# Optimization experiments

Measured on AMD Instinct MI355X. Metric: run time of the kernel, lower is better.

## Reference

```python
import jax, jax.numpy as jnp
import numpy as np

EPS = 1e-8

def _gauss_kernel(ks=7, sigma=7.0/6.0):
    x = np.arange(ks, dtype=np.float32) - ks // 2
    g = np.exp(-0.5 * (x / sigma) ** 2)
    g = g / g.sum()
    k = np.outer(g, g).astype(np.float32)
    return jnp.asarray(k.reshape(1, 1, ks, ks))

GK = _gauss_kernel()
SOBEL_X = jnp.asarray(np.array([[1, 0, -1], [2, 0, -2], [1, 0, -1]], dtype=np.float32).reshape(1, 1, 3, 3))
SOBEL_Y = jnp.transpose(SOBEL_X, (0, 1, 3, 2))


def _conv(x, k, pad):
    return jax.lax.conv_general_dilated(
        x, k, window_strides=(1, 1), padding=[(pad, pad), (pad, pad)],
        dimension_numbers=('NCHW', 'OIHW', 'NCHW'))


def _mscn(g):
    mu = _conv(g, GK, 3)
    sigma = jnp.sqrt(jnp.abs(_conv(g * g, GK, 3) - mu * mu + EPS))
    return (g - mu) / (sigma + EPS)


def _grad_mag(g):
    gx = _conv(g, SOBEL_X, 1)
    gy = _conv(g, SOBEL_Y, 1)
    return jnp.sqrt(gx * gx + gy * gy + EPS)


def _frfsim(D, R):
    w = jnp.array([0.2989, 0.587, 0.114], dtype=D.dtype).reshape(1, 3, 1, 1)
    Dg = jnp.sum(D * w, axis=1, keepdims=True)  # (B,1,H,W)
    Rg = jnp.sum(R * w, axis=1, keepdims=True)

    # per-sample SSIM-like constants from dynamic range of Dg (calculate_C)
    d = (jnp.max(Dg, axis=(2, 3), keepdims=True) -
         jnp.min(Dg, axis=(2, 3), keepdims=True))  # (B,1,1,1)
    CM = (0.01 * d) ** 2
    CD = CM / 2.0
    CG = (0.03 * d) ** 2
    CC = CG / 2.0

    # MSCN structure map
    Dm = _mscn(Dg)
    Rm = _mscn(Rg)
    SM = (2 * Dm * Rm + CM) / (Dm ** 2 + Rm ** 2 + CM)

    # dark-channel map
    Ddc = jnp.min(D, axis=1, keepdims=True) / 255.0
    Rdc = jnp.min(R, axis=1, keepdims=True) / 255.0
    SD = (2 * Ddc * Rdc + CD) / (Ddc ** 2 + Rdc ** 2 + CD + EPS)
    mean_SD = jnp.mean(SD, axis=(1, 2, 3))  # (B,)

    # HSV color map: s = (max-min+eps)/(max+eps), v = max, color = s*v
    def color(x):
        mx = jnp.max(x, axis=1, keepdims=True)
        mn = jnp.min(x, axis=1, keepdims=True)
        return ((mx - mn + EPS) / (mx + EPS)) * mx
    Dc = color(D)
    Rc = color(R)
    SC = (2 * Dc * Rc + CC) / (Dc ** 2 + Rc ** 2 + CC + EPS)

    # Sobel gradient map
    Dgr = _grad_mag(Dg)
    Rgr = _grad_mag(Rg)
    SG = (2 * Dgr * Rgr + CG) / (Dgr ** 2 + Rgr ** 2 + CG + EPS)

    # adaptive exponents from mean dark-channel similarity
    t1 = 0.85
    b1 = jnp.where((mean_SD > t1) & (mean_SD <= 1.0), 0.2,
                   jnp.where((mean_SD >= 0.0) & (mean_SD <= t1), 0.8, 0.5))
    b2 = jnp.where((mean_SD > t1) & (mean_SD <= 1.0), 0.8,
                   jnp.where((mean_SD >= 0.0) & (mean_SD <= t1), 0.2, 0.5))
    b1 = b1.astype(D.dtype).reshape(-1, 1, 1, 1)
    b2 = b2.astype(D.dtype).reshape(-1, 1, 1, 1)

    # safe_pow(base, b) == |base|^b (complex pow of |base|+0j, real part)
    frfsimmap = jnp.power(jnp.abs(SM * SD), b1) * jnp.power(SG * SC, b2)
    frfsimval = jnp.mean(jnp.abs(frfsimmap), axis=(1, 2, 3))  # (B,)
    return jnp.mean(frfsimval)  # == sum_i frfsimval_i / B


def setup_inputs() -> dict:
    key = jax.random.key(0)
    kD, kR = jax.random.split(key)
    B, H, W = 32, 512, 512
    D = jax.random.uniform(kD, (B, 3, H, W), dtype=jnp.float32)
    R = jax.random.uniform(kR, (B, 3, H, W), dtype=jnp.float32)
    return {"D": D, "R": R}


def reference(D, R):
    return _frfsim(D, R)
```

## Files before the change

### kernel.cpp

```cpp
#include <hip/hip_runtime.h>

#define EPSF  1e-8f
#define IMG_W 512
#define IMG_H 512
#define HWPX  (IMG_W*IMG_H)
#define NB    32

#define GW0 0.0125602730f
#define GW1 0.0788280293f
#define GW2 0.2372963577f
#define GW3 0.3426321149f

#define RCPF(x)  __builtin_amdgcn_rcpf(x)
#define SQRTF(x) __builtin_amdgcn_sqrtf(x)
#define LOG2F(x) __builtin_amdgcn_logf(x)
#define EXP2F(x) __builtin_amdgcn_exp2f(x)


__global__ void k_init(unsigned* __restrict__ minb, unsigned* __restrict__ maxb,
                       float* __restrict__ sdsum, float* __restrict__ cand) {
  int t = threadIdx.x;
  if (t < NB) { minb[t] = 0x7F7FFFFFu; maxb[t] = 0u; sdsum[t] = 0.f; }
  if (t < 3*NB) cand[t] = 0.f;
}

__global__ __launch_bounds__(256) void k_minmax(const float* __restrict__ D,
                                                unsigned* __restrict__ minb,
                                                unsigned* __restrict__ maxb) {
  const int b = blockIdx.y, chunk = blockIdx.x, tid = threadIdx.x;
  const float4* P0 = (const float4*)(D + (size_t)b * 3 * HWPX);
  const float4* P1 = P0 + HWPX/4;
  const float4* P2 = P1 + HWPX/4;
  const int i0 = chunk * 512 + tid;
  const int i1 = i0 + 256;
  float4 a0 = P0[i0], c0 = P1[i0], e0 = P2[i0];
  float4 a1 = P0[i1], c1 = P1[i1], e1 = P2[i1];
  float mn = __uint_as_float(0x7F7FFFFFu), mx = 0.f;
  float g;
  g = 0.2989f*a0.x + 0.587f*c0.x + 0.114f*e0.x; mn = fminf(mn,g); mx = fmaxf(mx,g);
  g = 0.2989f*a0.y + 0.587f*c0.y + 0.114f*e0.y; mn = fminf(mn,g); mx = fmaxf(mx,g);
  g = 0.2989f*a0.z + 0.587f*c0.z + 0.114f*e0.z; mn = fminf(mn,g); mx = fmaxf(mx,g);
  g = 0.2989f*a0.w + 0.587f*c0.w + 0.114f*e0.w; mn = fminf(mn,g); mx = fmaxf(mx,g);
  g = 0.2989f*a1.x + 0.587f*c1.x + 0.114f*e1.x; mn = fminf(mn,g); mx = fmaxf(mx,g);
  g = 0.2989f*a1.y + 0.587f*c1.y + 0.114f*e1.y; mn = fminf(mn,g); mx = fmaxf(mx,g);
  g = 0.2989f*a1.z + 0.587f*c1.z + 0.114f*e1.z; mn = fminf(mn,g); mx = fmaxf(mx,g);
  g = 0.2989f*a1.w + 0.587f*c1.w + 0.114f*e1.w; mn = fminf(mn,g); mx = fmaxf(mx,g);
  #pragma unroll
  for (int o = 32; o > 0; o >>= 1) {
    mn = fminf(mn, __shfl_down(mn, o, 64));
    mx = fmaxf(mx, __shfl_down(mx, o, 64));
  }
  __shared__ float smn[4], smx[4];
  if ((tid & 63) == 0) { smn[tid>>6] = mn; smx[tid>>6] = mx; }
  __syncthreads();
  if (tid == 0) {
    mn = fminf(fminf(smn[0],smn[1]), fminf(smn[2],smn[3]));
    mx = fmaxf(fmaxf(smx[0],smx[1]), fmaxf(smx[2],smx[3]));
    atomicMin(minb + b, __float_as_uint(mn));
    atomicMax(maxb + b, __float_as_uint(mx));
  }
}

#define TW 64
#define TH 32
#define HALO 3
#define SWP 72
#define SH  38
#define NCHUNK (SH*18)

__global__ __launch_bounds__(256) void k_main(const float* __restrict__ D, const float* __restrict__ R,
                                              const unsigned* __restrict__ minb,
                                              const unsigned* __restrict__ maxb,
                                              float* __restrict__ sdsum,
                                              float* __restrict__ cand) {
  __shared__ float sDg[SH][SWP];
  __shared__ float sRg[SH][SWP];
  __shared__ float sSD[TH][TW];
  __shared__ float sSC[TH][TW];

  const int tid = threadIdx.x;
  const int b   = blockIdx.z;
  const int tx0 = blockIdx.x * TW;
  const int ty0 = blockIdx.y * TH;

  const float dr = __uint_as_float(maxb[b]) - __uint_as_float(minb[b]);
  const float CM = (0.01f*dr)*(0.01f*dr);
  const float CD = 0.5f*CM;
  const float CG = (0.03f*dr)*(0.03f*dr);
  const float CC = 0.5f*CG;

  const float* D0 = D + (size_t)b*3*HWPX;
  const float* R0 = R + (size_t)b*3*HWPX;
  const float4* fD0 = (const float4*)D0;
  const float4* fD1 = fD0 + HWPX/4;
  const float4* fD2 = fD1 + HWPX/4;
  const float4* fR0 = (const float4*)R0;
  const float4* fR1 = fR0 + HWPX/4;
  const float4* fR2 = fR1 + HWPX/4;

  float sdacc = 0.f;

  const int cx0 = tx0 - 4;
  for (int j = tid; j < NCHUNK; j += 256) {
    const int r  = j / 18;
    const int c  = j - r*18;
    const int gy = ty0 - HALO + r;
    const int gx = cx0 + c*4;
    float4 dg4 = make_float4(0.f,0.f,0.f,0.f);
    float4 rg4 = make_float4(0.f,0.f,0.f,0.f);
    if ((unsigned)gy < IMG_H && gx >= 0 && gx < IMG_W) {
      const int o4 = gy*(IMG_W/4) + (gx >> 2);
      float4 d0 = fD0[o4], d1 = fD1[o4], d2 = fD2[o4];
      float4 r0 = fR0[o4], r1 = fR1[o4], r2 = fR2[o4];
      dg4.x = 0.2989f*d0.x + 0.587f*d1.x + 0.114f*d2.x;
      dg4.y = 0.2989f*d0.y + 0.587f*d1.y + 0.114f*d2.y;
      dg4.z = 0.2989f*d0.z + 0.587f*d1.z + 0.114f*d2.z;
      dg4.w = 0.2989f*d0.w + 0.587f*d1.w + 0.114f*d2.w;
      rg4.x = 0.2989f*r0.x + 0.587f*r1.x + 0.114f*r2.x;
      rg4.y = 0.2989f*r0.y + 0.587f*r1.y + 0.114f*r2.y;
      rg4.z = 0.2989f*r0.z + 0.587f*r1.z + 0.114f*r2.z;
      rg4.w = 0.2989f*r0.w + 0.587f*r1.w + 0.114f*r2.w;
      if (r >= HALO && r < HALO+TH && c >= 1 && c <= 16) {
        float4 sd4, sc4;
        #define MAPS(f) { \
          float dmn = fminf(fminf(d0.f,d1.f),d2.f); \
          float rmn = fminf(fminf(r0.f,r1.f),r2.f); \
          float a_ = dmn*(1.f/255.f), c_ = rmn*(1.f/255.f); \
          float sd = (2.f*a_*c_ + CD) * RCPF(a_*a_ + c_*c_ + CD + EPSF); \
          sd4.f = sd; sdacc += sd; \
          float dmx = fmaxf(fmaxf(d0.f,d1.f),d2.f); \
          float rmx = fmaxf(fmaxf(r0.f,r1.f),r2.f); \
          float dcol = ((dmx-dmn+EPSF) * RCPF(dmx+EPSF)) * dmx; \
          float rcol = ((rmx-rmn+EPSF) * RCPF(rmx+EPSF)) * rmx; \
          sc4.f = (2.f*dcol*rcol + CC) * RCPF(dcol*dcol + rcol*rcol + CC + EPSF); }
        MAPS(x) MAPS(y) MAPS(z) MAPS(w)
        #undef MAPS
        *(float4*)&sSD[r-HALO][(c-1)*4] = sd4;
        *(float4*)&sSC[r-HALO][(c-1)*4] = sc4;
      }
    }
    *(float4*)&sDg[r][c*4] = dg4;
    *(float4*)&sRg[r][c*4] = rg4;
  }
  __syncthreads();

  const int x   = tid & 63;
  const int yo0 = (tid >> 6) * 8;

  float whgD[7]={0}, whqD[7]={0}, whgR[7]={0}, whqR[7]={0};
  float wsxD[5]={0}, wsyD[5]={0}, wsxR[5]={0}, wsyR[5]={0};
  float a0 = 0.f, a1 = 0.f, a2 = 0.f;

  #pragma unroll
  for (int step = 0; step < 14; ++step) {
    const int r = yo0 + step;
    float vD[7], vR[7];
    #pragma unroll
    for (int j = 0; j < 7; ++j) { vD[j] = sDg[r][x+1+j]; vR[j] = sRg[r][x+1+j]; }
    float hgD, hqD, hgR, hqR;
    hgD = GW0*(vD[0]+vD[6]) + GW1*(vD[1]+vD[5]) + GW2*(vD[2]+vD[4]) + GW3*vD[3];
    hgR = GW0*(vR[0]+vR[6]) + GW1*(vR[1]+vR[5]) + GW2*(vR[2]+vR[4]) + GW3*vR[3];
    hqD = GW0*(vD[0]*vD[0]+vD[6]*vD[6]) + GW1*(vD[1]*vD[1]+vD[5]*vD[5])
        + GW2*(vD[2]*vD[2]+vD[4]*vD[4]) + GW3*vD[3]*vD[3];
    hqR = GW0*(vR[0]*vR[0]+vR[6]*vR[6]) + GW1*(vR[1]*vR[1]+vR[5]*vR[5])
        + GW2*(vR[2]*vR[2]+vR[4]*vR[4]) + GW3*vR[3]*vR[3];
    float sxD = vD[2]-vD[4], syD = vD[2]+2.f*vD[3]+vD[4];
    float sxR = vR[2]-vR[4], syR = vR[2]+2.f*vR[3]+vR[4];
    #pragma unroll
    for (int j = 0; j < 6; ++j) {
      whgD[j]=whgD[j+1]; whqD[j]=whqD[j+1]; whgR[j]=whgR[j+1]; whqR[j]=whqR[j+1];
    }
    whgD[6]=hgD; whqD[6]=hqD; whgR[6]=hgR; whqR[6]=hqR;
    #pragma unroll
    for (int j = 0; j < 4; ++j) {
      wsxD[j]=wsxD[j+1]; wsyD[j]=wsyD[j+1]; wsxR[j]=wsxR[j+1]; wsyR[j]=wsyR[j+1];
    }
    wsxD[4]=sxD; wsyD[4]=syD; wsxR[4]=sxR; wsyR[4]=syR;

    if (step >= 6) {
      const int yo = yo0 + step - 6;
      float muD, exD, muR, exR;
      muD = GW0*(whgD[0]+whgD[6]) + GW1*(whgD[1]+whgD[5]) + GW2*(whgD[2]+whgD[4]) + GW3*whgD[3];
      exD = GW0*(whqD[0]+whqD[6]) + GW1*(whqD[1]+whqD[5]) + GW2*(whqD[2]+whqD[4]) + GW3*whqD[3];
      muR = GW0*(whgR[0]+whgR[6]) + GW1*(whgR[1]+whgR[5]) + GW2*(whgR[2]+whgR[4]) + GW3*whgR[3];
      exR = GW0*(whqR[0]+whqR[6]) + GW1*(whqR[1]+whqR[5]) + GW2*(whqR[2]+whqR[4]) + GW3*whqR[3];
      float v0D = sDg[yo+HALO][x+4];
      float v0R = sRg[yo+HALO][x+4];
      float sigD = SQRTF(fabsf(exD - muD*muD + EPSF));
      float sigR = SQRTF(fabsf(exR - muR*muR + EPSF));
      float Dm = (v0D - muD) * RCPF(sigD + EPSF);
      float Rm = (v0R - muR) * RCPF(sigR + EPSF);
      float SM = (2.f*Dm*Rm + CM) * RCPF(Dm*Dm + Rm*Rm + CM);
      float gxD = wsxD[0] + 2.f*wsxD[1] + wsxD[2];
      float gyD = wsyD[0] - wsyD[2];
      float gxR = wsxR[0] + 2.f*wsxR[1] + wsxR[2];
      float gyR = wsyR[0] - wsyR[2];
      float GD = SQRTF(gxD*gxD + gyD*gyD + EPSF);
      float GR = SQRTF(gxR*gxR + gyR*gyR + EPSF);
      float SG = (2.f*GD*GR + CG) * RCPF(GD*GD + GR*GR + CG + EPSF);
      float SDv = sSD[yo][x];
      float SCv = sSC[yo][x];
      float m1 = fabsf(SM * SDv);
      float m2 = SG * SCv;
      float l1 = LOG2F(m1);
      float l2 = LOG2F(m2);
      a0 += EXP2F(0.2f*l1 + 0.8f*l2);
      a1 += EXP2F(0.8f*l1 + 0.2f*l2);
      a2 += EXP2F(0.5f*l1 + 0.5f*l2);
    }
  }

  #pragma unroll
  for (int o = 32; o > 0; o >>= 1) {
    sdacc += __shfl_down(sdacc, o, 64);
    a0    += __shfl_down(a0,    o, 64);
    a1    += __shfl_down(a1,    o, 64);
    a2    += __shfl_down(a2,    o, 64);
  }
  __shared__ float red[4][4];
  const int w = tid >> 6;
  if ((tid & 63) == 0) { red[w][0]=sdacc; red[w][1]=a0; red[w][2]=a1; red[w][3]=a2; }
  __syncthreads();
  if (tid < 4) {
    float t = red[0][tid]+red[1][tid]+red[2][tid]+red[3][tid];
    if (tid == 0) atomicAdd(sdsum + b, t);
    else          atomicAdd(cand + (tid-1)*NB + b, t);
  }
}

__global__ void k_final(const float* __restrict__ sdsum, const float* __restrict__ cand,
                        float* __restrict__ out) {
  const int t = threadIdx.x;
  float v = 0.f;
  if (t < NB) {
    float meanSD = sdsum[t] * (1.f/(float)HWPX);
    float c;
    if      (meanSD > 0.85f && meanSD <= 1.0f)  c = cand[0*NB + t];
    else if (meanSD >= 0.f  && meanSD <= 0.85f) c = cand[1*NB + t];
    else                                        c = cand[2*NB + t];
    v = c;
  }
  #pragma unroll
  for (int o = 32; o > 0; o >>= 1) v += __shfl_down(v, o, 64);
  if (t == 0) out[0] = v * (1.f/8388608.f);
}

extern "C" void kernel_launch(void* const* d_in, const int* in_sizes, int n_in,
                              void* d_out, int out_size, void* d_ws, size_t ws_size,
                              hipStream_t stream) {
  (void)in_sizes; (void)n_in; (void)out_size; (void)ws_size;
  const float* D = (const float*)d_in[0];
  const float* R = (const float*)d_in[1];
  float* out = (float*)d_out;
  unsigned* minb  = (unsigned*)d_ws;
  unsigned* maxb  = minb + NB;
  float*    sdsum = (float*)(maxb + NB);
  float*    cand  = sdsum + NB;

  k_init  <<<1, 128, 0, stream>>>(minb, maxb, sdsum, cand);
  k_minmax<<<dim3(128, NB), 256, 0, stream>>>(D, minb, maxb);
  k_main  <<<dim3(IMG_W/TW, IMG_H/TH, NB), 256, 0, stream>>>(D, R, minb, maxb, sdsum, cand);
  k_final <<<1, 64, 0, stream>>>(sdsum, cand, out);
}
```

Measured before the change: 330.8 us.

## Split D/R stencil passes to cut registers; replace min/max atomics with two-stage reduction

The fused stencil loop that kept D and R sliding windows live together is split into two passes. The first computes the D MSCN values and gradient magnitudes into small per-thread arrays, and the second processes R and combines them. This lowers peak register pressure so more waves can be resident, at the cost of re-reading the D values from shared memory in a separate pass. The per-image min/max atomics are also replaced by per-chunk partial writes plus a small reduction kernel, which adds one extra launch.

```diff
diff --git a/kernel.cpp b/kernel.cpp
--- a/kernel.cpp
+++ b/kernel.cpp
@@ -5,6 +5,7 @@
 #define IMG_H 512
 #define HWPX  (IMG_W*IMG_H)
 #define NB    32
+#define NCHK  128
 
 #define GW0 0.0125602730f
 #define GW1 0.0788280293f
@@ -17,16 +18,15 @@
 #define EXP2F(x) __builtin_amdgcn_exp2f(x)
 
 
-__global__ void k_init(unsigned* __restrict__ minb, unsigned* __restrict__ maxb,
-                       float* __restrict__ sdsum, float* __restrict__ cand) {
+__global__ void k_init(float* __restrict__ sdsum, float* __restrict__ cand) {
   int t = threadIdx.x;
-  if (t < NB) { minb[t] = 0x7F7FFFFFu; maxb[t] = 0u; sdsum[t] = 0.f; }
+  if (t < NB) sdsum[t] = 0.f;
   if (t < 3*NB) cand[t] = 0.f;
 }
 
 __global__ __launch_bounds__(256) void k_minmax(const float* __restrict__ D,
-                                                unsigned* __restrict__ minb,
-                                                unsigned* __restrict__ maxb) {
+                                                float* __restrict__ mnp,
+                                                float* __restrict__ mxp) {
   const int b = blockIdx.y, chunk = blockIdx.x, tid = threadIdx.x;
   const float4* P0 = (const float4*)(D + (size_t)b * 3 * HWPX);
   const float4* P1 = P0 + HWPX/4;
@@ -56,8 +56,27 @@
   if (tid == 0) {
     mn = fminf(fminf(smn[0],smn[1]), fminf(smn[2],smn[3]));
     mx = fmaxf(fmaxf(smx[0],smx[1]), fmaxf(smx[2],smx[3]));
-    atomicMin(minb + b, __float_as_uint(mn));
-    atomicMax(maxb + b, __float_as_uint(mx));
+    mnp[b*NCHK + chunk] = mn;
+    mxp[b*NCHK + chunk] = mx;
+  }
+}
+
+__global__ void k_red(const float* __restrict__ mnp, const float* __restrict__ mxp,
+                      unsigned* __restrict__ minb, unsigned* __restrict__ maxb) {
+  const int b = blockIdx.x, t = threadIdx.x;
+  float mn = mnp[b*NCHK + t];
+  float mx = mxp[b*NCHK + t];
+  #pragma unroll
+  for (int o = 32; o > 0; o >>= 1) {
+    mn = fminf(mn, __shfl_down(mn, o, 64));
+    mx = fmaxf(mx, __shfl_down(mx, o, 64));
+  }
+  __shared__ float smn[2], smx[2];
+  if ((t & 63) == 0) { smn[t>>6] = mn; smx[t>>6] = mx; }
+  __syncthreads();
+  if (t == 0) {
+    minb[b] = __float_as_uint(fminf(smn[0], smn[1]));
+    maxb[b] = __float_as_uint(fmaxf(smx[0], smx[1]));
   }
 }
 
@@ -89,12 +108,10 @@
   const float CG = (0.03f*dr)*(0.03f*dr);
   const float CC = 0.5f*CG;
 
-  const float* D0 = D + (size_t)b*3*HWPX;
-  const float* R0 = R + (size_t)b*3*HWPX;
-  const float4* fD0 = (const float4*)D0;
+  const float4* fD0 = (const float4*)(D + (size_t)b*3*HWPX);
   const float4* fD1 = fD0 + HWPX/4;
   const float4* fD2 = fD1 + HWPX/4;
-  const float4* fR0 = (const float4*)R0;
+  const float4* fR0 = (const float4*)(R + (size_t)b*3*HWPX);
   const float4* fR1 = fR0 + HWPX/4;
   const float4* fR2 = fR1 + HWPX/4;
 
@@ -147,66 +164,91 @@
   const int x   = tid & 63;
   const int yo0 = (tid >> 6) * 8;
 
-  float whgD[7]={0}, whqD[7]={0}, whgR[7]={0}, whqR[7]={0};
-  float wsxD[5]={0}, wsyD[5]={0}, wsxR[5]={0}, wsyR[5]={0};
+  float nD[8], gD[8];
+  {
+    float whg[7]={0,0,0,0,0,0,0}, whq[7]={0,0,0,0,0,0,0};
+    float wsx[3]={0,0,0}, wsy[3]={0,0,0};
+    #pragma unroll
+    for (int st = 0; st < 14; ++st) {
+      const int r = yo0 + st;
+      float v[7];
+      #pragma unroll
+      for (int j = 0; j < 7; ++j) v[j] = sDg[r][x+1+j];
+      float hg = GW0*(v[0]+v[6]) + GW1*(v[1]+v[5]) + GW2*(v[2]+v[4]) + GW3*v[3];
+      float hq = GW0*(v[0]*v[0]+v[6]*v[6]) + GW1*(v[1]*v[1]+v[5]*v[5])
+               + GW2*(v[2]*v[2]+v[4]*v[4]) + GW3*v[3]*v[3];
+      #pragma unroll
+      for (int j = 0; j < 6; ++j) { whg[j]=whg[j+1]; whq[j]=whq[j+1]; }
+      whg[6]=hg; whq[6]=hq;
+      wsx[0]=wsx[1]; wsx[1]=wsx[2]; wsx[2]=v[2]-v[4];
+      wsy[0]=wsy[1]; wsy[1]=wsy[2]; wsy[2]=v[2]+2.f*v[3]+v[4];
+      if (st >= 4 && st < 12) {
+        float gx = wsx[0] + 2.f*wsx[1] + wsx[2];
+        float gy = wsy[0] - wsy[2];
+        gD[st-4] = SQRTF(gx*gx + gy*gy + EPSF);
+      }
+      if (st >= 6) {
+        const int k  = st - 6;
+        const int ya = yo0 + k;
+        float mu = GW0*(whg[0]+whg[6]) + GW1*(whg[1]+whg[5]) + GW2*(whg[2]+whg[4]) + GW3*whg[3];
+        float ex = GW0*(whq[0]+whq[6]) + GW1*(whq[1]+whq[5]) + GW2*(whq[2]+whq[4]) + GW3*whq[3];
+        float v0 = sDg[ya+HALO][x+4];
+        float sig = SQRTF(fabsf(ex - mu*mu + EPSF));
+        nD[k] = (v0 - mu) * RCPF(sig + EPSF);
+      }
+    }
+  }
+
   float a0 = 0.f, a1 = 0.f, a2 = 0.f;
-
-  #pragma unroll
-  for (int step = 0; step < 14; ++step) {
-    const int r = yo0 + step;
-    float vD[7], vR[7];
+  {
+    float whg[7]={0,0,0,0,0,0,0}, whq[7]={0,0,0,0,0,0,0};
+    float wsx[3]={0,0,0}, wsy[3]={0,0,0};
+    float grr[2]={0,0};
     #pragma unroll
-    for (int j = 0; j < 7; ++j) { vD[j] = sDg[r][x+1+j]; vR[j] = sRg[r][x+1+j]; }
-    float hgD, hqD, hgR, hqR;
-    hgD = GW0*(vD[0]+vD[6]) + GW1*(vD[1]+vD[5]) + GW2*(vD[2]+vD[4]) + GW3*vD[3];
-    hgR = GW0*(vR[0]+vR[6]) + GW1*(vR[1]+vR[5]) + GW2*(vR[2]+vR[4]) + GW3*vR[3];
-    hqD = GW0*(vD[0]*vD[0]+vD[6]*vD[6]) + GW1*(vD[1]*vD[1]+vD[5]*vD[5])
-        + GW2*(vD[2]*vD[2]+vD[4]*vD[4]) + GW3*vD[3]*vD[3];
-    hqR = GW0*(vR[0]*vR[0]+vR[6]*vR[6]) + GW1*(vR[1]*vR[1]+vR[5]*vR[5])
-        + GW2*(vR[2]*vR[2]+vR[4]*vR[4]) + GW3*vR[3]*vR[3];
-    float sxD = vD[2]-vD[4], syD = vD[2]+2.f*vD[3]+vD[4];
-    float sxR = vR[2]-vR[4], syR = vR[2]+2.f*vR[3]+vR[4];
-    #pragma unroll
-    for (int j = 0; j < 6; ++j) {
-      whgD[j]=whgD[j+1]; whqD[j]=whqD[j+1]; whgR[j]=whgR[j+1]; whqR[j]=whqR[j+1];
-    }
-    whgD[6]=hgD; whqD[6]=hqD; whgR[6]=hgR; whqR[6]=hqR;
-    #pragma unroll
-    for (int j = 0; j < 4; ++j) {
-      wsxD[j]=wsxD[j+1]; wsyD[j]=wsyD[j+1]; wsxR[j]=wsxR[j+1]; wsyR[j]=wsyR[j+1];
-    }
-    wsxD[4]=sxD; wsyD[4]=syD; wsxR[4]=sxR; wsyR[4]=syR;
-
-    if (step >= 6) {
-      const int yo = yo0 + step - 6;
-      float muD, exD, muR, exR;
-      muD = GW0*(whgD[0]+whgD[6]) + GW1*(whgD[1]+whgD[5]) + GW2*(whgD[2]+whgD[4]) + GW3*whgD[3];
-      exD = GW0*(whqD[0]+whqD[6]) + GW1*(whqD[1]+whqD[5]) + GW2*(whqD[2]+whqD[4]) + GW3*whqD[3];
-      muR = GW0*(whgR[0]+whgR[6]) + GW1*(whgR[1]+whgR[5]) + GW2*(whgR[2]+whgR[4]) + GW3*whgR[3];
-      exR = GW0*(whqR[0]+whqR[6]) + GW1*(whqR[1]+whqR[5]) + GW2*(whqR[2]+whqR[4]) + GW3*whqR[3];
-      float v0D = sDg[yo+HALO][x+4];
-      float v0R = sRg[yo+HALO][x+4];
-      float sigD = SQRTF(fabsf(exD - muD*muD + EPSF));
-      float sigR = SQRTF(fabsf(exR - muR*muR + EPSF));
-      float Dm = (v0D - muD) * RCPF(sigD + EPSF);
-      float Rm = (v0R - muR) * RCPF(sigR + EPSF);
-      float SM = (2.f*Dm*Rm + CM) * RCPF(Dm*Dm + Rm*Rm + CM);
-      float gxD = wsxD[0] + 2.f*wsxD[1] + wsxD[2];
-      float gyD = wsyD[0] - wsyD[2];
-      float gxR = wsxR[0] + 2.f*wsxR[1] + wsxR[2];
-      float gyR = wsyR[0] - wsyR[2];
-      float GD = SQRTF(gxD*gxD + gyD*gyD + EPSF);
-      float GR = SQRTF(gxR*gxR + gyR*gyR + EPSF);
-      float SG = (2.f*GD*GR + CG) * RCPF(GD*GD + GR*GR + CG + EPSF);
-      float SDv = sSD[yo][x];
-      float SCv = sSC[yo][x];
-      float m1 = fabsf(SM * SDv);
-      float m2 = SG * SCv;
-      float l1 = LOG2F(m1);
-      float l2 = LOG2F(m2);
-      a0 += EXP2F(0.2f*l1 + 0.8f*l2);
-      a1 += EXP2F(0.8f*l1 + 0.2f*l2);
-      a2 += EXP2F(0.5f*l1 + 0.5f*l2);
+    for (int st = 0; st < 14; ++st) {
+      const int r = yo0 + st;
+      float v[7];
+      #pragma unroll
+      for (int j = 0; j < 7; ++j) v[j] = sRg[r][x+1+j];
+      float hg = GW0*(v[0]+v[6]) + GW1*(v[1]+v[5]) + GW2*(v[2]+v[4]) + GW3*v[3];
+      float hq = GW0*(v[0]*v[0]+v[6]*v[6]) + GW1*(v[1]*v[1]+v[5]*v[5])
+               + GW2*(v[2]*v[2]+v[4]*v[4]) + GW3*v[3]*v[3];
+      #pragma unroll
+      for (int j = 0; j < 6; ++j) { whg[j]=whg[j+1]; whq[j]=whq[j+1]; }
+      whg[6]=hg; whq[6]=hq;
+      wsx[0]=wsx[1]; wsx[1]=wsx[2]; wsx[2]=v[2]-v[4];
+      wsy[0]=wsy[1]; wsy[1]=wsy[2]; wsy[2]=v[2]+2.f*v[3]+v[4];
+
+      float GRuse = grr[st & 1];
+
+      if (st >= 4 && st < 12) {
+        float gx = wsx[0] + 2.f*wsx[1] + wsx[2];
+        float gy = wsy[0] - wsy[2];
+        grr[st & 1] = SQRTF(gx*gx + gy*gy + EPSF);
+      }
+
+      if (st >= 6) {
+        const int k  = st - 6;
+        const int ya = yo0 + k;
+        float mu = GW0*(whg[0]+whg[6]) + GW1*(whg[1]+whg[5]) + GW2*(whg[2]+whg[4]) + GW3*whg[3];
+        float ex = GW0*(whq[0]+whq[6]) + GW1*(whq[1]+whq[5]) + GW2*(whq[2]+whq[4]) + GW3*whq[3];
+        float v0 = sRg[ya+HALO][x+4];
+        float sig = SQRTF(fabsf(ex - mu*mu + EPSF));
+        float Rm = (v0 - mu) * RCPF(sig + EPSF);
+        float Dm = nD[k];
+        float SM = (2.f*Dm*Rm + CM) * RCPF(Dm*Dm + Rm*Rm + CM);
+        float GDv = gD[k];
+        float SG = (2.f*GDv*GRuse + CG) * RCPF(GDv*GDv + GRuse*GRuse + CG + EPSF);
+        float SDv = sSD[ya][x];
+        float SCv = sSC[ya][x];
+        float m1 = fabsf(SM * SDv);
+        float m2 = SG * SCv;
+        float l1 = LOG2F(m1);
+        float l2 = LOG2F(m2);
+        a0 += EXP2F(0.2f*l1 + 0.8f*l2);
+        a1 += EXP2F(0.8f*l1 + 0.2f*l2);
+        a2 += EXP2F(0.5f*l1 + 0.5f*l2);
+      }
     }
   }
 
@@ -256,9 +298,12 @@
   unsigned* maxb  = minb + NB;
   float*    sdsum = (float*)(maxb + NB);
   float*    cand  = sdsum + NB;
-
-  k_init  <<<1, 128, 0, stream>>>(minb, maxb, sdsum, cand);
-  k_minmax<<<dim3(128, NB), 256, 0, stream>>>(D, minb, maxb);
+  float*    mnp   = cand + 3*NB;
+  float*    mxp   = mnp + NB*NCHK;
+
+  k_init  <<<1, 128, 0, stream>>>(sdsum, cand);
+  k_minmax<<<dim3(NCHK, NB), 256, 0, stream>>>(D, mnp, mxp);
+  k_red   <<<NB, 128, 0, stream>>>(mnp, mxp, minb, maxb);
   k_main  <<<dim3(IMG_W/TW, IMG_H/TH, NB), 256, 0, stream>>>(D, R, minb, maxb, sdsum, cand);
   k_final <<<1, 64, 0, stream>>>(sdsum, cand, out);
 }
```

Measured after the change: 320.2 us. 3.2% less time.
